# Kernel tuning notes

Measured on AMD Instinct MI355X. Metric: run time of the kernel, lower is better.

The kernel has to match this reference:

```python
import jax, jax.numpy as jnp
import numpy as np

POINT_NB = 256
DILATION = 1
EPS = 1e-4  # pad mask value used by shiftFeat (0.0001)


def _shift(where, f, d):
    """Replicate-pad shift of f:[B,C,H,W]; returns shifted features and
    channel-averaged validity mask [B,1,H,W] (1 inside, EPS in pad region)."""
    B, C, H, W = f.shape
    m = jnp.ones((B, 1, H, W), dtype=f.dtype)
    if where == 'none':
        return f, m
    if where == 'left':
        fs = jnp.concatenate([f[..., d:], jnp.broadcast_to(f[..., -1:], (B, C, H, d))], axis=-1)
        m = m.at[..., -d:].set(EPS)
    elif where == 'right':
        fs = jnp.concatenate([jnp.broadcast_to(f[..., :1], (B, C, H, d)), f[..., :-d]], axis=-1)
        m = m.at[..., :d].set(EPS)
    elif where == 'top':
        fs = jnp.concatenate([f[:, :, d:, :], jnp.broadcast_to(f[:, :, -1:, :], (B, C, d, W))], axis=2)
        m = m.at[:, :, -d:, :].set(EPS)
    elif where == 'bot':
        fs = jnp.concatenate([jnp.broadcast_to(f[:, :, :1, :], (B, C, d, W)), f[:, :, :-d, :]], axis=2)
        m = m.at[:, :, :d, :].set(EPS)
    else:
        raise ValueError(where)
    return fs, m


def _cos_sim(f1, f2, m1, m2):
    # sim = sum(f1*f2*m1*m2, C) / (||m1*f1|| * ||m2*f2||); masks are [B,1,H,W], m>0
    num = (m1 * m2) * jnp.sum(f1 * f2, axis=1, keepdims=True)
    den = (m1 * jnp.sqrt(jnp.sum(f1 * f1, axis=1, keepdims=True))) * \
          (m2 * jnp.sqrt(jnp.sum(f2 * f2, axis=1, keepdims=True)))
    return num / den


def _total_sim(features, d):
    f1, m1 = _shift('right', features, d)
    f2, m2 = _shift('left', features, d)
    horiz = _cos_sim(f1, f2, m1, m2)
    f1, m1 = _shift('top', features, d)
    f2, m2 = _shift('bot', features, d)
    verti = _cos_sim(f1, f2, m1, m2)
    return (horiz + verti) * 0.5  # [B,1,H,W]


def setup_inputs() -> dict:
    key = jax.random.key(0)
    features = jax.random.normal(key, (16, 256, 56, 56), dtype=jnp.float32)
    return {"features": features}


def reference(features):
    B, C, H, W = features.shape
    sim = _total_sim(features, DILATION)            # [B,1,H,W]
    flat = sim.reshape(B, H * W)                    # [B,HW]
    vals, idx = jax.lax.top_k(flat, POINT_NB)       # [B,K]
    ycoord = idx // W
    xcoord = idx % W
    # gather feature vectors at selected points: [B,C,HW] -> [B,K,C]
    feat_flat = features.reshape(B, C, H * W)
    point_feat = jnp.take_along_axis(feat_flat, idx[:, None, :], axis=2)
    point_feat = jnp.transpose(point_feat, (0, 2, 1))
    return point_feat, vals, ycoord, xcoord
```

## Files before the change

kernel.cpp:

```cpp
#include <hip/hip_runtime.h>

#define NB 16
#define NC 256
#define NH 56
#define NW 56
#define NHW (NH * NW)
#define NK 256
#define TK_THREADS 1024
#define CAP 1024

#define BR 4
#define RS 6
#define CS 16
#define CHALF 128
#define NCHUNK_H (CHALF / CS)
#define CHUNK16 (CS * RS * NW / 4)
#define NBAND (NH / BR)
#define P1_BLOCKS (NB * NBAND * 2)
#define NQ (BR * (NW / 4))
#define MAPS (NB * NHW)

__device__ inline unsigned int flip_f32(float f) {
    unsigned int u = __float_as_uint(f);
    return (u & 0x80000000u) ? ~u : (u | 0x80000000u);
}
__device__ inline float unflip_f32(unsigned int u) {
    u = (u & 0x80000000u) ? (u ^ 0x80000000u) : ~u;
    return __uint_as_float(u);
}

__global__ void __launch_bounds__(256)
pass1_kernel(const float* __restrict__ f, float* __restrict__ maps) {
    __shared__ __align__(16) float buf[2][CS * RS * NW];
    __shared__ float redbuf[NQ][4][12];

    int bid = blockIdx.x;
    int sb = (bid & 7) * (P1_BLOCKS / 8) + (bid >> 3);
    int b = sb / 28;
    int rem0 = sb - b * 28;
    int band = rem0 >> 1;
    int chh = rem0 & 1;
    int y0 = band * BR;
    int tid = threadIdx.x;
    const float* fb = f + (size_t)b * NC * NHW + (size_t)chh * CHALF * NHW;

    auto stage = [&](int ci, float* dst) {
        int c0 = ci * CS;
#pragma unroll
        for (int i = 0; i < 6; ++i) {
            int k = tid + 256 * i;
            if (k < CHUNK16) {
                int ch = k / (RS * 14);
                int rem = k - ch * (RS * 14);
                int rl = rem / 14;
                int xk = rem - rl * 14;
                int rg = y0 - 1 + rl;
                rg = rg < 0 ? 0 : (rg > NH - 1 ? NH - 1 : rg);
                const float* src = fb + (size_t)(c0 + ch) * NHW + rg * NW + xk * 4;
                __builtin_amdgcn_global_load_lds(
                    (const __attribute__((address_space(1))) void*)src,
                    (__attribute__((address_space(3))) void*)(dst + k * 4),
                    16, 0, 0);
            }
        }
    };

    int chg = tid / NQ;
    int quad = tid - chg * NQ;
    int r = quad / 14, qx = quad - r * 14, x0 = qx * 4;
    int xl = x0 ? x0 - 1 : 0;
    int xr = (x0 + 4 < NW) ? x0 + 4 : NW - 1;

    float n0 = 0.f, n1 = 0.f, n2 = 0.f, n3 = 0.f;
    float h0 = 0.f, h1 = 0.f, h2 = 0.f, h3 = 0.f;
    float w0 = 0.f, w1 = 0.f, w2 = 0.f, w3 = 0.f;

    stage(0, buf[0]);
    __syncthreads();
    for (int ci = 0; ci < NCHUNK_H; ++ci) {
        if (ci + 1 < NCHUNK_H) stage(ci + 1, buf[(ci + 1) & 1]);
        if (tid < 4 * NQ) {
            const float* sbf = buf[ci & 1];
#pragma unroll
            for (int c = 0; c < 4; ++c) {
                const float* Bm = sbf + (chg * 4 + c) * (RS * NW) + (r + 1) * NW;
                float4 v = *(const float4*)(Bm + x0);
                float  l = Bm[xl];
                float  rr = Bm[xr];
                float4 u = *(const float4*)(Bm + NW + x0);
                float4 d = *(const float4*)(Bm - NW + x0);
                n0 += v.x * v.x; n1 += v.y * v.y; n2 += v.z * v.z; n3 += v.w * v.w;
                h0 += l * v.y;   h1 += v.x * v.z; h2 += v.y * v.w; h3 += v.z * rr;
                w0 += u.x * d.x; w1 += u.y * d.y; w2 += u.z * d.z; w3 += u.w * d.w;
            }
        }
        __syncthreads();
    }

    if (tid < 4 * NQ) {
        float* rb = redbuf[quad][chg];
        rb[0] = n0; rb[1] = n1; rb[2]  = n2; rb[3]  = n3;
        rb[4] = h0; rb[5] = h1; rb[6]  = h2; rb[7]  = h3;
        rb[8] = w0; rb[9] = w1; rb[10] = w2; rb[11] = w3;
    }
    __syncthreads();

    float* mbase = maps + (size_t)chh * 3 * MAPS;
    for (int oi = tid; oi < NQ * 12; oi += 256) {
        int q = oi / 12, comp = oi - q * 12;
        float acc = 0.f;
#pragma unroll
        for (int g = 0; g < 4; ++g) acc += redbuf[q][g][comp];
        int r2 = q / 14, qx2 = q - r2 * 14;
        int j = comp & 3;
        float* m = mbase + (size_t)(comp >> 2) * MAPS;
        m[((size_t)b * NH + y0 + r2) * NW + qx2 * 4 + j] = acc;
    }
}

__global__ void __launch_bounds__(256)
sim_kernel(const float* __restrict__ maps, unsigned int* __restrict__ sv) {
    int pix = blockIdx.x * 256 + threadIdx.x;
    if (pix >= NB * NHW) return;
    int b = pix / NHW, i = pix - b * NHW;
    const float* na  = maps + (size_t)b * NHW;
    const float* ha  = na + MAPS;
    const float* va  = na + 2 * (size_t)MAPS;
    const float* nb2 = na + 3 * (size_t)MAPS;
    const float* hb2 = na + 4 * (size_t)MAPS;
    const float* vb2 = na + 5 * (size_t)MAPS;

    int y = i / NW, x = i - y * NW;
    int xl = (x > 0) ? x - 1 : 0;
    int xr = (x < NW - 1) ? x + 1 : NW - 1;
    int yu = (y < NH - 1) ? y + 1 : NH - 1;
    int yd = (y > 0) ? y - 1 : 0;
    int il = y * NW + xl, ir = y * NW + xr;
    int iu = yu * NW + x, id = yd * NW + x;

    float nl = na[il] + nb2[il];
    float nr = na[ir] + nb2[ir];
    float nu = na[iu] + nb2[iu];
    float nd = na[id] + nb2[id];
    float h = ha[i] + hb2[i], v = va[i] + vb2[i];
    float s = 0.5f * (h / (sqrtf(nl) * sqrtf(nr)) + v / (sqrtf(nu) * sqrtf(nd)));
    sv[pix] = flip_f32(s);
}

__global__ void __launch_bounds__(TK_THREADS)
topk_kernel(const unsigned int* __restrict__ sv, int* __restrict__ idx_out,
            float* __restrict__ vals_out, float* __restrict__ y_out,
            float* __restrict__ x_out) {
    __shared__ unsigned int svals[NHW];
    __shared__ unsigned int hist16[16][256];
    __shared__ unsigned long long cand[CAP];
    __shared__ unsigned int sh_prefix, sh_mask;
    __shared__ int sh_cnt, sh_above, sh_setS, sh_done;

    const int b = blockIdx.x;
    const int tid = threadIdx.x;
    const int lane = tid & 63;
    const int wv = tid >> 6;
    const unsigned int* svb = sv + (size_t)b * NHW;

    for (int i = tid; i < NHW; i += TK_THREADS) svals[i] = svb[i];
    if (tid == 0) { sh_prefix = 0u; sh_mask = 0u; sh_above = 0; sh_done = 0; }

    int shift = 24;
    for (int stage = 0; stage < 4; ++stage) {
        __syncthreads();
        if (sh_done) break;
        for (int i = tid; i < 16 * 256; i += TK_THREADS) ((unsigned int*)hist16)[i] = 0u;
        __syncthreads();
        unsigned int pfx = sh_prefix, msk = sh_mask;
        for (int i = tid; i < NHW; i += TK_THREADS) {
            unsigned int v = svals[i];
            if ((v & msk) == pfx) atomicAdd(&hist16[wv][(v >> shift) & 255u], 1u);
        }
        __syncthreads();
        if (tid < 64) {
            int l = tid;
            unsigned int kneed = (unsigned int)(NK - sh_above);
            unsigned int h0 = 0, h1 = 0, h2 = 0, h3 = 0;
#pragma unroll
            for (int w = 0; w < 16; ++w) {
                h0 += hist16[w][4 * l + 0]; h1 += hist16[w][4 * l + 1];
                h2 += hist16[w][4 * l + 2]; h3 += hist16[w][4 * l + 3];
            }
            unsigned int lsum = h0 + h1 + h2 + h3;
            unsigned int s = lsum;
#pragma unroll
            for (int d = 1; d < 64; d <<= 1) {
                unsigned int t = __shfl_down(s, d);
                s += (l + d < 64) ? t : 0u;
            }
            unsigned int above_l = s - lsum;
            unsigned int suf3 = above_l + h3;
            unsigned int suf2 = suf3 + h2;
            unsigned int suf1 = suf2 + h1;
            unsigned int suf0 = suf1 + h0;
            bool has = (suf0 >= kneed);
            unsigned long long bal = __ballot(has);
            int hl = 63 - __clzll(bal);
            if (l == hl) {
                int c; unsigned int above, hc;
                if (suf3 >= kneed)      { c = 4 * l + 3; above = above_l; hc = h3; }
                else if (suf2 >= kneed) { c = 4 * l + 2; above = suf3;    hc = h2; }
                else if (suf1 >= kneed) { c = 4 * l + 1; above = suf2;    hc = h1; }
                else                    { c = 4 * l + 0; above = suf1;    hc = h0; }
                sh_above += (int)above;
                sh_setS = (int)hc;
                sh_prefix |= ((unsigned int)c) << shift;
                sh_mask   |= 255u << shift;
                if (sh_above + sh_setS <= 512 || shift == 0) sh_done = 1;
            }
        }
        shift -= 8;
    }
    __syncthreads();

    if (tid == 0) sh_cnt = 0;
    __syncthreads();
    unsigned int T = sh_prefix;
    for (int i = tid; i < NHW; i += TK_THREADS) {
        unsigned int v = svals[i];
        bool keep = (v >= T);
        unsigned long long m = __ballot(keep);
        int basep = 0;
        if (lane == 0) basep = atomicAdd(&sh_cnt, __popcll(m));
        basep = __shfl(basep, 0);
        if (keep) {
            int pos = basep + __popcll(m & ((1ull << lane) - 1ull));
            if (pos < CAP)
                cand[pos] = ((unsigned long long)v << 32) |
                            (unsigned long long)(0xFFFFFFFFu - (unsigned int)i);
        }
    }
    __syncthreads();
    int nc = sh_cnt; if (nc > CAP) nc = CAP;
    const int NS = (nc <= 512) ? 512 : CAP;
    for (int i = tid; i < NS; i += TK_THREADS) if (i >= nc) cand[i] = 0ull;
    __syncthreads();

    for (int k = 2; k <= NS; k <<= 1) {
        for (int j = k >> 1; j > 0; j >>= 1) {
            for (int i = tid; i < NS; i += TK_THREADS) {
                int ixj = i ^ j;
                if (ixj > i) {
                    unsigned long long a = cand[i], c2 = cand[ixj];
                    bool sw = ((i & k) == 0) ? (a < c2) : (a > c2);
                    if (sw) { cand[i] = c2; cand[ixj] = a; }
                }
            }
            __syncthreads();
        }
    }

    if (tid < NK) {
        unsigned long long kk = cand[tid];
        unsigned int lo = (unsigned int)(kk & 0xFFFFFFFFull);
        int idx = (int)(0xFFFFFFFFu - lo);
        float val = unflip_f32((unsigned int)(kk >> 32));
        int o = b * NK + tid;
        idx_out[o] = idx;
        vals_out[o] = val;
        y_out[o] = (float)(idx / NW);
        x_out[o] = (float)(idx % NW);
    }
}

__global__ void __launch_bounds__(256)
gather_kernel(const float* __restrict__ f, const int* __restrict__ idx,
              float* __restrict__ out) {
    int bid = blockIdx.x;
    int xcd = bid & 7, i = bid >> 3;
    int b = xcd + 8 * (i & 1);
    int kg = i >> 1;
    int c = threadIdx.x;
    const float* fb = f + (size_t)b * NC * NHW + (size_t)c * NHW;
#pragma unroll
    for (int j = 0; j < 4; ++j) {
        int k = kg * 4 + j;
        int p = idx[b * NK + k];
        out[((size_t)b * NK + k) * NC + c] = fb[p];
    }
}

extern "C" void kernel_launch(void* const* d_in, const int* in_sizes, int n_in,
                              void* d_out, int out_size, void* d_ws, size_t ws_size,
                              hipStream_t stream) {
    const float* f = (const float*)d_in[0];

    float* out_feat = (float*)d_out;
    float* out_vals = out_feat + (size_t)NB * NK * NC;
    float* out_y    = out_vals + (size_t)NB * NK;
    float* out_x    = out_y    + (size_t)NB * NK;

    float* maps = (float*)d_ws;
    unsigned int* sv = (unsigned int*)(maps + 6 * (size_t)MAPS);
    int* idx = (int*)(sv + MAPS);

    pass1_kernel<<<P1_BLOCKS, 256, 0, stream>>>(f, maps);
    sim_kernel<<<(NB * NHW + 255) / 256, 256, 0, stream>>>(maps, sv);
    topk_kernel<<<NB, TK_THREADS, 0, stream>>>(sv, idx, out_vals, out_y, out_x);
    gather_kernel<<<NB * NK / 4, 256, 0, stream>>>(f, idx, out_feat);
}
```

Measured before the change: 43.14 us.

## Use 12-bit radix select passes and rank-count selection instead of bitonic sort

```diff
diff --git a/kernel.cpp b/kernel.cpp
--- a/kernel.cpp
+++ b/kernel.cpp
@@ -6,7 +6,6 @@
 #define NW 56
 #define NHW (NH * NW)
 #define NK 256
-#define TK_THREADS 1024
 #define CAP 1024
 
 #define BR 4
@@ -147,15 +146,16 @@
     sv[pix] = flip_f32(s);
 }
 
-__global__ void __launch_bounds__(TK_THREADS)
+__global__ void __launch_bounds__(1024)
 topk_kernel(const unsigned int* __restrict__ sv, int* __restrict__ idx_out,
             float* __restrict__ vals_out, float* __restrict__ y_out,
             float* __restrict__ x_out) {
     __shared__ unsigned int svals[NHW];
-    __shared__ unsigned int hist16[16][256];
+    __shared__ unsigned int hist[4096];
+    __shared__ unsigned int wtot[16];
     __shared__ unsigned long long cand[CAP];
     __shared__ unsigned int sh_prefix, sh_mask;
-    __shared__ int sh_cnt, sh_above, sh_setS, sh_done;
+    __shared__ int sh_above, sh_setS, sh_done, sh_cnt;
 
     const int b = blockIdx.x;
     const int tid = threadIdx.x;
@@ -163,66 +163,62 @@
     const int wv = tid >> 6;
     const unsigned int* svb = sv + (size_t)b * NHW;
 
-    for (int i = tid; i < NHW; i += TK_THREADS) svals[i] = svb[i];
+    for (int i = tid; i < NHW; i += 1024) svals[i] = svb[i];
     if (tid == 0) { sh_prefix = 0u; sh_mask = 0u; sh_above = 0; sh_done = 0; }
 
-    int shift = 24;
-    for (int stage = 0; stage < 4; ++stage) {
-        __syncthreads();
+    const int shifts[3] = {20, 8, 0};
+    const unsigned int wmasks[3] = {0xFFFu, 0xFFFu, 0xFFu};
+    for (int st = 0; st < 3; ++st) {
+        __syncthreads();
+        int kneed = NK - sh_above;
         if (sh_done) break;
-        for (int i = tid; i < 16 * 256; i += TK_THREADS) ((unsigned int*)hist16)[i] = 0u;
+        for (int i = tid; i < 4096; i += 1024) hist[i] = 0u;
         __syncthreads();
         unsigned int pfx = sh_prefix, msk = sh_mask;
-        for (int i = tid; i < NHW; i += TK_THREADS) {
+        int shift = shifts[st];
+        unsigned int wmask = wmasks[st];
+        for (int i = tid; i < NHW; i += 1024) {
             unsigned int v = svals[i];
-            if ((v & msk) == pfx) atomicAdd(&hist16[wv][(v >> shift) & 255u], 1u);
-        }
-        __syncthreads();
-        if (tid < 64) {
-            int l = tid;
-            unsigned int kneed = (unsigned int)(NK - sh_above);
-            unsigned int h0 = 0, h1 = 0, h2 = 0, h3 = 0;
-#pragma unroll
-            for (int w = 0; w < 16; ++w) {
-                h0 += hist16[w][4 * l + 0]; h1 += hist16[w][4 * l + 1];
-                h2 += hist16[w][4 * l + 2]; h3 += hist16[w][4 * l + 3];
-            }
-            unsigned int lsum = h0 + h1 + h2 + h3;
-            unsigned int s = lsum;
-#pragma unroll
-            for (int d = 1; d < 64; d <<= 1) {
-                unsigned int t = __shfl_down(s, d);
-                s += (l + d < 64) ? t : 0u;
-            }
-            unsigned int above_l = s - lsum;
-            unsigned int suf3 = above_l + h3;
-            unsigned int suf2 = suf3 + h2;
-            unsigned int suf1 = suf2 + h1;
-            unsigned int suf0 = suf1 + h0;
-            bool has = (suf0 >= kneed);
-            unsigned long long bal = __ballot(has);
-            int hl = 63 - __clzll(bal);
-            if (l == hl) {
-                int c; unsigned int above, hc;
-                if (suf3 >= kneed)      { c = 4 * l + 3; above = above_l; hc = h3; }
-                else if (suf2 >= kneed) { c = 4 * l + 2; above = suf3;    hc = h2; }
-                else if (suf1 >= kneed) { c = 4 * l + 1; above = suf2;    hc = h1; }
-                else                    { c = 4 * l + 0; above = suf1;    hc = h0; }
-                sh_above += (int)above;
-                sh_setS = (int)hc;
-                sh_prefix |= ((unsigned int)c) << shift;
-                sh_mask   |= 255u << shift;
-                if (sh_above + sh_setS <= 512 || shift == 0) sh_done = 1;
-            }
-        }
-        shift -= 8;
+            if ((v & msk) == pfx) atomicAdd(&hist[(v >> shift) & wmask], 1u);
+        }
+        __syncthreads();
+        unsigned int b0 = hist[4 * tid], b1 = hist[4 * tid + 1];
+        unsigned int b2 = hist[4 * tid + 2], b3 = hist[4 * tid + 3];
+        unsigned int lsum = b0 + b1 + b2 + b3;
+        unsigned int s = lsum;
+#pragma unroll
+        for (int d = 1; d < 64; d <<= 1) {
+            unsigned int t2 = __shfl_down(s, d);
+            s += (lane + d < 64) ? t2 : 0u;
+        }
+        if (lane == 0) wtot[wv] = s;
+        __syncthreads();
+        unsigned int wabove = 0;
+        for (int w = wv + 1; w < 16; ++w) wabove += wtot[w];
+        unsigned int thr_above = wabove + (s - lsum);
+        unsigned int suf3 = thr_above + b3;
+        unsigned int suf2 = suf3 + b2;
+        unsigned int suf1 = suf2 + b1;
+        unsigned int suf0 = suf1 + b0;
+        if (suf0 >= (unsigned int)kneed && thr_above < (unsigned int)kneed) {
+            int c; unsigned int above, hc;
+            if (suf3 >= (unsigned int)kneed)      { c = 4 * tid + 3; above = thr_above; hc = b3; }
+            else if (suf2 >= (unsigned int)kneed) { c = 4 * tid + 2; above = suf3;      hc = b2; }
+            else if (suf1 >= (unsigned int)kneed) { c = 4 * tid + 1; above = suf2;      hc = b1; }
+            else                                  { c = 4 * tid + 0; above = suf1;      hc = b0; }
+            sh_above += (int)above;
+            sh_setS = (int)hc;
+            sh_prefix = pfx | ((unsigned int)c << shift);
+            sh_mask = msk | (wmask << shift);
+            if (sh_above + sh_setS <= CAP || st == 2) sh_done = 1;
+        }
     }
     __syncthreads();
 
     if (tid == 0) sh_cnt = 0;
     __syncthreads();
     unsigned int T = sh_prefix;
-    for (int i = tid; i < NHW; i += TK_THREADS) {
+    for (int i = tid; i < NHW; i += 1024) {
         unsigned int v = svals[i];
         bool keep = (v >= T);
         unsigned long long m = __ballot(keep);
@@ -238,34 +234,21 @@
     }
     __syncthreads();
     int nc = sh_cnt; if (nc > CAP) nc = CAP;
-    const int NS = (nc <= 512) ? 512 : CAP;
-    for (int i = tid; i < NS; i += TK_THREADS) if (i >= nc) cand[i] = 0ull;
-    __syncthreads();
-
-    for (int k = 2; k <= NS; k <<= 1) {
-        for (int j = k >> 1; j > 0; j >>= 1) {
-            for (int i = tid; i < NS; i += TK_THREADS) {
-                int ixj = i ^ j;
-                if (ixj > i) {
-                    unsigned long long a = cand[i], c2 = cand[ixj];
-                    bool sw = ((i & k) == 0) ? (a < c2) : (a > c2);
-                    if (sw) { cand[i] = c2; cand[ixj] = a; }
-                }
-            }
-            __syncthreads();
-        }
-    }
-
-    if (tid < NK) {
-        unsigned long long kk = cand[tid];
-        unsigned int lo = (unsigned int)(kk & 0xFFFFFFFFull);
-        int idx = (int)(0xFFFFFFFFu - lo);
-        float val = unflip_f32((unsigned int)(kk >> 32));
-        int o = b * NK + tid;
-        idx_out[o] = idx;
-        vals_out[o] = val;
-        y_out[o] = (float)(idx / NW);
-        x_out[o] = (float)(idx % NW);
+
+    if (tid < nc) {
+        unsigned long long my = cand[tid];
+        int rank = 0;
+        for (int i = 0; i < nc; ++i) rank += (cand[i] > my);
+        if (rank < NK) {
+            unsigned int lo = (unsigned int)(my & 0xFFFFFFFFull);
+            int idx = (int)(0xFFFFFFFFu - lo);
+            float val = unflip_f32((unsigned int)(my >> 32));
+            int o = b * NK + rank;
+            idx_out[o] = idx;
+            vals_out[o] = val;
+            y_out[o] = (float)(idx / NW);
+            x_out[o] = (float)(idx % NW);
+        }
     }
 }
 
@@ -302,6 +285,6 @@
 
     pass1_kernel<<<P1_BLOCKS, 256, 0, stream>>>(f, maps);
     sim_kernel<<<(NB * NHW + 255) / 256, 256, 0, stream>>>(maps, sv);
-    topk_kernel<<<NB, TK_THREADS, 0, stream>>>(sv, idx, out_vals, out_y, out_x);
+    topk_kernel<<<NB, 1024, 0, stream>>>(sv, idx, out_vals, out_y, out_x);
     gather_kernel<<<NB * NK / 4, 256, 0, stream>>>(f, idx, out_feat);
 }
```

Result: faster. 37.97 us (-12.0%).
